# Kernel tuning notes

Hardware: AMD Instinct MI355X
Metric: run time of the kernel (lower is better)

The kernel has to match this reference:

```python
import jax, jax.numpy as jnp
import numpy as np

REPLACE = 4
REMAIN = 32
EPS = 1e-12


def _l2norm(x, axis):
    return x / jnp.maximum(jnp.linalg.norm(x, axis=axis, keepdims=True), EPS)


def setup_inputs() -> dict:
    key = jax.random.key(0)
    ks = jax.random.split(key, 16)
    B, d = 4096, 64
    n_users, n_entities, n_items = 100000, 200000, 50000
    K, n_cans, n_rel = 64, 64, 100
    return {
        "users": jax.random.randint(ks[0], (B,), 0, n_users),
        "items": jax.random.randint(ks[1], (B,), 0, n_items),
        "kg_neighbors": jax.random.randint(ks[2], (n_items, K), 0, n_entities),
        "all_candidates": jax.random.randint(ks[3], (n_rel, n_cans), 0, n_entities),
        "neighbor_relations": jax.random.randint(ks[4], (n_items, K), 0, n_rel),
        "user_all_embeddings": jax.random.normal(ks[5], (n_users, d), jnp.float32),
        "entity_all_embeddings": jax.random.normal(ks[6], (n_entities, d), jnp.float32),
        "item_embeddings": jax.random.normal(ks[7], (B, d), jnp.float32),
        "ui_W": jax.random.normal(ks[8], (2 * d, d), jnp.float32) / np.sqrt(2 * d),
        "ui_b": jnp.zeros((d,), jnp.float32),
        "e1_W": jax.random.normal(ks[9], (d, d), jnp.float32) / np.sqrt(d),
        "e1_b": jnp.zeros((d,), jnp.float32),
        "e2_W": jax.random.normal(ks[10], (d, d), jnp.float32) / np.sqrt(d),
        "e2_b": jnp.zeros((d,), jnp.float32),
    }


def reference(users, items, kg_neighbors, all_candidates, neighbor_relations,
              user_all_embeddings, entity_all_embeddings, item_embeddings,
              ui_W, ui_b, e1_W, e1_b, e2_W, e2_b):
    B = users.shape[0]
    d = user_all_embeddings.shape[1]
    idx_dtype = kg_neighbors.dtype

    neighbors = kg_neighbors[items]                      # [B, K]
    users_e = user_all_embeddings[users]                 # [B, d]
    ui_e = _l2norm(jnp.concatenate([users_e, item_embeddings], axis=1) @ ui_W + ui_b, 1)  # [B, d]

    # Step 1: score neighbors, pick top replace_num
    ne = _l2norm(entity_all_embeddings[neighbors] @ e1_W + e1_b, 2)   # [B, K, d]
    scores1 = jnp.einsum('bd,bkd->bk', ui_e, ne)
    logits1 = jax.nn.softmax(scores1, axis=1)
    step1_prob, step1_idx = jax.lax.top_k(logits1, REPLACE)          # [B, R]
    replaced = jnp.take_along_axis(neighbors, step1_idx, axis=1)     # [B, R]
    sel_rel = jnp.take_along_axis(neighbor_relations[items], step1_idx, axis=1)
    cf_kg1 = kg_neighbors.at[items[:, None], step1_idx].set(
        jnp.zeros((B, REPLACE), idx_dtype))
    ap1 = jnp.log(jnp.mean(step1_prob, axis=1))                      # [B]

    # Step 2: candidate pruning + sampling
    cands = all_candidates[sel_rel]                                  # [B, R, C]
    cands_e = entity_all_embeddings[cands]                           # [B, R, C, d]
    scores2 = jnp.einsum('bd,brcd->brc', users_e, cands_e)
    _, remain_idx = jax.lax.top_k(scores2, REMAIN)                   # [B, R, M]
    cands = jnp.take_along_axis(cands, remain_idx, axis=2).reshape(B * REPLACE, REMAIN)

    replaced_e = _l2norm(entity_all_embeddings[replaced] @ e1_W + e1_b, 2)
    replaced_e = replaced_e.reshape(B * REPLACE, d)
    cands_e2 = _l2norm(entity_all_embeddings[cands] @ e2_W + e2_b, 2)  # [BR, M, d]
    ui_rep = jnp.repeat(ui_e, REPLACE, axis=0)                         # [BR, d]
    s2 = jnp.einsum('nd,nmd->nm', ui_rep * replaced_e, cands_e2)       # [BR, M]
    logp2 = jax.nn.log_softmax(s2, axis=1)

    skey = jax.random.key(42)
    step2_idx = jax.random.categorical(skey, logp2, axis=1)           # [BR]
    rows = jnp.arange(B * REPLACE)
    step2_prob = jnp.exp(logp2[rows, step2_idx]).reshape(B, REPLACE)
    sel_ent = cands[rows, step2_idx].reshape(B, REPLACE)
    cf_kg2 = kg_neighbors.at[items[:, None], step1_idx].set(sel_ent.astype(idx_dtype))
    ap2 = jnp.log(jnp.mean(step1_prob, axis=1)) + jnp.log(jnp.mean(step2_prob, axis=1))
    return (cf_kg1, ap1, cf_kg2, ap2)
```

## Files before the change

### kernel.cpp

```cpp
#include <hip/hip_runtime.h>
#include <stdint.h>

#define EPS_NORM 1e-12f
#define F32_TINY 1.17549435e-38f

static __device__ __forceinline__ int rfl(int v) {
  return __builtin_amdgcn_readfirstlane(v);
}

__device__ __forceinline__ void threefry2x32(uint32_t k0, uint32_t k1,
                                             uint32_t x0, uint32_t x1,
                                             uint32_t& o0, uint32_t& o1) {
  uint32_t ks2 = k0 ^ k1 ^ 0x1BD11BDAu;
  x0 += k0; x1 += k1;
#define TF_ROT(r) { x0 += x1; x1 = (x1 << (r)) | (x1 >> (32 - (r))); x1 ^= x0; }
  TF_ROT(13) TF_ROT(15) TF_ROT(26) TF_ROT(6)
  x0 += k1; x1 += ks2 + 1u;
  TF_ROT(17) TF_ROT(29) TF_ROT(16) TF_ROT(24)
  x0 += ks2; x1 += k0 + 2u;
  TF_ROT(13) TF_ROT(15) TF_ROT(26) TF_ROT(6)
  x0 += k0; x1 += k1 + 3u;
  TF_ROT(17) TF_ROT(29) TF_ROT(16) TF_ROT(24)
  x0 += k1; x1 += ks2 + 4u;
  TF_ROT(13) TF_ROT(15) TF_ROT(26) TF_ROT(6)
  x0 += ks2; x1 += k0 + 5u;
#undef TF_ROT
  o0 = x0; o1 = x1;
}

#define PERM_IDX(p) ((((p) & 7) << 3) | ((p) >> 3))

__global__ __launch_bounds__(256) void k_phase1(
    const float* __restrict__ E, const int* __restrict__ allc,
    const float* __restrict__ W1, const float* __restrict__ b1,
    const float* __restrict__ W2, const float* __restrict__ b2,
    const float* __restrict__ U, const int* __restrict__ users,
    const float* __restrict__ Iemb, const float* __restrict__ uiW,
    const float* __restrict__ uib, const int* __restrict__ kg,
    float* __restrict__ T1, float* __restrict__ T2c,
    float* __restrict__ uiE, float* __restrict__ out0, float* __restrict__ out2,
    int* __restrict__ wkg2) {
  __shared__ float SM[8192];
  const int blk = blockIdx.x, tid = threadIdx.x;
  const int wv = tid >> 6, lane = tid & 63;
  const int NT1B = 782, NT2B = 25, NUIB = 256;
  if (blk < NT1B + NT2B) {
    const bool isT1 = blk < NT1B;
    {
      const float* W = isT1 ? W1 : W2;
      for (int idx = tid; idx < 4096; idx += 256) {
        int k = idx >> 6, c = idx & 63;
        int cg = c & 7, ci = c >> 3;
        SM[k * 64 + ((ci >> 2) * 8 + cg) * 4 + (ci & 3)] = W[idx];
      }
    }
    __syncthreads();
    const int rg = lane >> 3, cg = lane & 7;
    const int sub = lane >> 5, r = lane & 31;
    const float* bias = isT1 ? b1 : b2;
    float bv[8];
#pragma unroll
    for (int ci = 0; ci < 8; ++ci) bv[ci] = bias[ci * 8 + cg];
    float* eTw = SM + 4096 + wv * 1024;
    const float4* eT4 = reinterpret_cast<const float4*>(eTw);
    const float4* W4 = reinterpret_cast<const float4*>(SM);
#pragma unroll 1
    for (int t = 0; t < 2; ++t) {
      int batch = (isT1 ? blk : blk - NT1B) * 2 + t;
      int rbase = batch * 128 + wv * 32;
      if (isT1 && rbase >= 200000) continue;
      int srow = isT1 ? (rbase + r) : allc[rbase + r];
      const float4* Er = reinterpret_cast<const float4*>(E + (size_t)srow * 64);
      float4 a0 = Er[sub * 4 + 0], a1 = Er[sub * 4 + 1];
      float4 a2 = Er[sub * 4 + 2], a3 = Er[sub * 4 + 3];
      float4 a4 = Er[8 + sub * 4 + 0], a5 = Er[8 + sub * 4 + 1];
      float4 a6 = Er[8 + sub * 4 + 2], a7 = Er[8 + sub * 4 + 3];
      float y[4][8];
#pragma unroll
      for (int ri = 0; ri < 4; ++ri)
#pragma unroll
        for (int ci = 0; ci < 8; ++ci) y[ri][ci] = 0.f;
      {
        float ev[16] = {a0.x, a0.y, a0.z, a0.w, a1.x, a1.y, a1.z, a1.w,
                        a2.x, a2.y, a2.z, a2.w, a3.x, a3.y, a3.z, a3.w};
#pragma unroll
        for (int kk = 0; kk < 16; ++kk)
          eTw[(sub * 16 + kk) * 32 + r] = ev[kk];
#pragma unroll 8
        for (int kk = 0; kk < 32; ++kk) {
          float4 e4 = eT4[kk * 8 + rg];
          float4 wa = W4[kk * 16 + cg];
          float4 wb = W4[kk * 16 + 8 + cg];
          float ev4[4] = {e4.x, e4.y, e4.z, e4.w};
          float wv8[8] = {wa.x, wa.y, wa.z, wa.w, wb.x, wb.y, wb.z, wb.w};
#pragma unroll
          for (int ri = 0; ri < 4; ++ri)
#pragma unroll
            for (int ci = 0; ci < 8; ++ci)
              y[ri][ci] = fmaf(ev4[ri], wv8[ci], y[ri][ci]);
        }
      }
      {
        float ev[16] = {a4.x, a4.y, a4.z, a4.w, a5.x, a5.y, a5.z, a5.w,
                        a6.x, a6.y, a6.z, a6.w, a7.x, a7.y, a7.z, a7.w};
#pragma unroll
        for (int kk = 0; kk < 16; ++kk)
          eTw[(sub * 16 + kk) * 32 + r] = ev[kk];
#pragma unroll 8
        for (int kk = 0; kk < 32; ++kk) {
          float4 e4 = eT4[kk * 8 + rg];
          float4 wa = W4[(32 + kk) * 16 + cg];
          float4 wb = W4[(32 + kk) * 16 + 8 + cg];
          float ev4[4] = {e4.x, e4.y, e4.z, e4.w};
          float wv8[8] = {wa.x, wa.y, wa.z, wa.w, wb.x, wb.y, wb.z, wb.w};
#pragma unroll
          for (int ri = 0; ri < 4; ++ri)
#pragma unroll
            for (int ci = 0; ci < 8; ++ci)
              y[ri][ci] = fmaf(ev4[ri], wv8[ci], y[ri][ci]);
        }
      }
#pragma unroll
      for (int ri = 0; ri < 4; ++ri)
#pragma unroll
        for (int ci = 0; ci < 8; ++ci)
          y[ri][ci] = __fadd_rn(y[ri][ci], bv[ci]);
#pragma unroll
      for (int ri = 0; ri < 4; ++ri) {
        float A0 = __fadd_rn(__fmul_rn(y[ri][0], y[ri][0]),
                             __fmul_rn(y[ri][4], y[ri][4]));
        float A1 = __fadd_rn(__fmul_rn(y[ri][1], y[ri][1]),
                             __fmul_rn(y[ri][5], y[ri][5]));
        float A2 = __fadd_rn(__fmul_rn(y[ri][2], y[ri][2]),
                             __fmul_rn(y[ri][6], y[ri][6]));
        float A3 = __fadd_rn(__fmul_rn(y[ri][3], y[ri][3]),
                             __fmul_rn(y[ri][7], y[ri][7]));
        float B0 = __fadd_rn(A0, A2), B1 = __fadd_rn(A1, A3);
        float C = __fadd_rn(B0, B1);
        C = __fadd_rn(C, __shfl_xor(C, 4));
        C = __fadd_rn(C, __shfl_xor(C, 2));
        C = __fadd_rn(C, __shfl_xor(C, 1));
        float denom = fmaxf(sqrtf(C), EPS_NORM);
        int row = rbase + rg * 4 + ri;
        if (isT1) {
          float4* drow = reinterpret_cast<float4*>(T1 + (size_t)row * 64 + cg * 8);
          drow[0] = make_float4(y[ri][0] / denom, y[ri][1] / denom,
                                y[ri][2] / denom, y[ri][3] / denom);
          drow[1] = make_float4(y[ri][4] / denom, y[ri][5] / denom,
                                y[ri][6] / denom, y[ri][7] / denom);
        } else {
          float* drow = T2c + (size_t)row * 64;
#pragma unroll
          for (int ci = 0; ci < 8; ++ci) drow[ci * 8 + cg] = y[ri][ci] / denom;
        }
      }
    }
  } else if (blk < NT1B + NT2B + NUIB) {
    int ub = blk - (NT1B + NT2B);
    for (int i = tid; i < 8192; i += 256) SM[i] = uiW[i];
    __syncthreads();
    float bl = uib[lane];
#pragma unroll 1
    for (int t = 0; t < 4; ++t) {
      int b = ub * 16 + wv * 4 + t;
      int usr = rfl(users[b]);
      const float* ur = U + (size_t)usr * 64;
      const float* ir = Iemb + (size_t)b * 64;
      float y = 0.f;
#pragma unroll
      for (int k = 0; k < 64; ++k) y = fmaf(ur[k], SM[k * 64 + lane], y);
#pragma unroll
      for (int k = 0; k < 64; ++k) y = fmaf(ir[k], SM[(64 + k) * 64 + lane], y);
      y += bl;
      float ss = y * y;
#pragma unroll
      for (int off = 32; off; off >>= 1) ss += __shfl_xor(ss, off);
      float yn = y / fmaxf(sqrtf(ss), EPS_NORM);
      uiE[(size_t)b * 64 + lane] = yn;
    }
  } else {
    const int4* kg4 = reinterpret_cast<const int4*>(kg);
    float4* o4 = reinterpret_cast<float4*>(out0);
    float4* o24 = reinterpret_cast<float4*>(out2);
    int4* wz = reinterpret_cast<int4*>(wkg2);
    int4 z; z.x = 0; z.y = 0; z.z = 0; z.w = 0;
    for (int i = (blk - 1063) * 256 + tid; i < 800000; i += 200 * 256) {
      int4 v = kg4[i];
      float4 f = make_float4((float)v.x, (float)v.y, (float)v.z, (float)v.w);
      o4[i] = f;
      o24[i] = f;
      wz[i] = z;
    }
  }
}

__global__ __launch_bounds__(256) void k_step(
    const int* __restrict__ items, const int* __restrict__ users,
    const int* __restrict__ kg, const int* __restrict__ nrel,
    const int* __restrict__ allc, const float* __restrict__ E,
    const float* __restrict__ T1, const float* __restrict__ T2c,
    const float* __restrict__ uiE, const float* __restrict__ U,
    float* __restrict__ out0, float* __restrict__ ap1_out,
    int* __restrict__ s1i_g, float* __restrict__ lmp1,
    float* __restrict__ p2, int* __restrict__ wkg2) {
  __shared__ int s1_idx_sh[4], s1_rel_sh[4], s1_ent_sh[4];
  __shared__ int kept_sh[128];
  const int tid = threadIdx.x, wv = tid >> 6, lane = tid & 63;
  const int b = blockIdx.x;
  const int item = rfl(items[b]);
  if (wv == 0) {
    int nb = kg[(size_t)item * 64 + lane];
    const float4* R = reinterpret_cast<const float4*>(T1 + (size_t)nb * 64);
    float yn[64];
#pragma unroll
    for (int p4 = 0; p4 < 16; ++p4) {
      float4 v = R[p4];
      yn[PERM_IDX(4 * p4 + 0)] = v.x;
      yn[PERM_IDX(4 * p4 + 1)] = v.y;
      yn[PERM_IDX(4 * p4 + 2)] = v.z;
      yn[PERM_IDX(4 * p4 + 3)] = v.w;
    }
    const float4* Ur = reinterpret_cast<const float4*>(uiE + (size_t)b * 64);
    float D[32];
#pragma unroll
    for (int i4 = 0; i4 < 8; ++i4) {
      float4 ua = Ur[i4], ub = Ur[i4 + 8];
      float uav[4] = {ua.x, ua.y, ua.z, ua.w};
      float ubv[4] = {ub.x, ub.y, ub.z, ub.w};
#pragma unroll
      for (int t = 0; t < 4; ++t) {
        int i = i4 * 4 + t;
        D[i] = __fadd_rn(__fmul_rn(yn[i], uav[t]), __fmul_rn(yn[i + 32], ubv[t]));
      }
    }
#pragma unroll
    for (int i = 0; i < 16; ++i) D[i] = __fadd_rn(D[i], D[i + 16]);
#pragma unroll
    for (int i = 0; i < 8; ++i)  D[i] = __fadd_rn(D[i], D[i + 8]);
#pragma unroll
    for (int i = 0; i < 4; ++i)  D[i] = __fadd_rn(D[i], D[i + 4]);
#pragma unroll
    for (int i = 0; i < 2; ++i)  D[i] = __fadd_rn(D[i], D[i + 2]);
    float s = __fadd_rn(D[0], D[1]);
    float m = s;
#pragma unroll
    for (int off = 32; off; off >>= 1) m = fmaxf(m, __shfl_xor(m, off));
    float ex = expf(s - m);
    float sum = ex;
#pragma unroll
    for (int off = 32; off; off >>= 1) sum += __shfl_xor(sum, off);
    float p = ex / sum;
    int rank = 0;
    for (int k2 = 0; k2 < 64; ++k2) {
      float pv = __shfl(p, k2);
      rank += (pv > p || (pv == p && k2 < lane)) ? 1 : 0;
    }
    float acc = 0.f;
#pragma unroll
    for (int rr = 0; rr < 4; ++rr) {
      unsigned long long msk = __ballot(rank == rr);
      int src = __ffsll(msk) - 1;
      acc += __shfl(p, src);
    }
    float lm = logf(acc * 0.25f);
    if (lane == 0) { ap1_out[b] = lm; lmp1[b] = lm; }
    if (rank < 4) {
      s1_idx_sh[rank] = lane;
      s1_ent_sh[rank] = nb;
      s1_rel_sh[rank] = nrel[(size_t)item * 64 + lane];
      s1i_g[b * 4 + rank] = lane;
      out0[(size_t)item * 64 + lane] = 0.0f;
    }
  }
  __syncthreads();
  const int n = b * 4 + wv;
  const int rel = rfl(s1_rel_sh[wv]);
  const int repl = rfl(s1_ent_sh[wv]);
  const int colsel = rfl(s1_idx_sh[wv]);
  {
    int usr = rfl(users[b]);
    int ent = allc[rel * 64 + lane];
    const float* ur = U + (size_t)usr * 64;
    const float4* e4 = reinterpret_cast<const float4*>(E + (size_t)ent * 64);
    float s = 0.f;
#pragma unroll
    for (int j4 = 0; j4 < 16; ++j4) {
      float4 t = e4[j4];
      s = fmaf(ur[4 * j4 + 0], t.x, s);
      s = fmaf(ur[4 * j4 + 1], t.y, s);
      s = fmaf(ur[4 * j4 + 2], t.z, s);
      s = fmaf(ur[4 * j4 + 3], t.w, s);
    }
    int rank = 0;
    for (int k2 = 0; k2 < 64; ++k2) {
      float sv = __shfl(s, k2);
      rank += (sv > s || (sv == s && k2 < lane)) ? 1 : 0;
    }
    if (rank < 32) kept_sh[wv * 32 + rank] = (lane << 18) | ent;
  }
  {
    int m = lane & 31;
    int pk = kept_sh[wv * 32 + m];
    int c = pk >> 18;
    int ent = pk & 0x3FFFF;
    float q = uiE[(size_t)b * 64 + PERM_IDX(lane)] * T1[(size_t)repl * 64 + lane];
    const float4* c4 = reinterpret_cast<const float4*>(
        T2c + ((size_t)rel * 64 + c) * 64);
    float s = 0.f;
#pragma unroll
    for (int j4 = 0; j4 < 16; ++j4) {
      float4 t = c4[j4];
      s = fmaf(__shfl(q, PERM_IDX(4 * j4 + 0)), t.x, s);
      s = fmaf(__shfl(q, PERM_IDX(4 * j4 + 1)), t.y, s);
      s = fmaf(__shfl(q, PERM_IDX(4 * j4 + 2)), t.z, s);
      s = fmaf(__shfl(q, PERM_IDX(4 * j4 + 3)), t.w, s);
    }
    float mx = s;
#pragma unroll
    for (int off = 1; off < 32; off <<= 1) mx = fmaxf(mx, __shfl_xor(mx, off));
    float shv = s - mx;
    float se = expf(shv);
    float sum = se;
#pragma unroll
    for (int off = 1; off < 32; off <<= 1) sum += __shfl_xor(sum, off);
    float logp = shv - logf(sum);
    uint32_t h0, h1;
    threefry2x32(0u, 42u, 0u, (uint32_t)(n * 32 + m), h0, h1);
    uint32_t bits = h0 ^ h1;
    float u0 = __uint_as_float((bits >> 9) | 0x3F800000u) - 1.0f;
    float uu = fmaxf(u0, F32_TINY);
    float g = -logf(-logf(uu));
    float z = g + logp;
    float bz = z; int bm = m;
#pragma unroll
    for (int off = 1; off < 32; off <<= 1) {
      float oz = __shfl_xor(bz, off);
      int om = __shfl_xor(bm, off);
      if (oz > bz || (oz == bz && om < bm)) { bz = oz; bm = om; }
    }
    if (lane == bm) {
      p2[n] = expf(logp);
      atomicMax(&wkg2[(size_t)item * 64 + colsel], ((b + 1) << 18) | ent);
    }
  }
}

__global__ __launch_bounds__(256) void k_fin2(
    const int* __restrict__ items, const int* __restrict__ s1_idx,
    const int* __restrict__ wkg2, const float* __restrict__ p2,
    const float* __restrict__ lmp1,
    float* __restrict__ out2, float* __restrict__ out3, int N, int B) {
  int i = blockIdx.x * 256 + threadIdx.x;
  if (i < N) {
    int b = i >> 2;
    int item = items[b];
    int col = s1_idx[i];
    int v = wkg2[(size_t)item * 64 + col];
    out2[(size_t)item * 64 + col] = (float)(v & 0x3FFFF);
  }
  if (i < B) {
    float a = ((p2[i * 4] + p2[i * 4 + 1]) + p2[i * 4 + 2]) + p2[i * 4 + 3];
    out3[i] = lmp1[i] + logf(a * 0.25f);
  }
}

__global__ __launch_bounds__(256) void k_init(const int* __restrict__ kg,
                                              float* __restrict__ out0,
                                              int* __restrict__ wkg2, int n) {
  int i = blockIdx.x * 256 + threadIdx.x;
  if (i < n) { int v = kg[i]; out0[i] = (float)v; wkg2[i] = v; }
}

__device__ __forceinline__ void transform_row(const float4* __restrict__ Er,
                                              const float* __restrict__ W,
                                              const float* __restrict__ bias,
                                              float (&yn)[64]) {
  float y[64];
#pragma unroll
  for (int j = 0; j < 64; ++j) y[j] = 0.f;
  float4 c0 = Er[0], c1 = Er[1], c2 = Er[2], c3 = Er[3];
#pragma unroll 1
  for (int cc = 0; cc < 4; ++cc) {
    float4 n0, n1, n2, n3;
    if (cc < 3) { n0 = Er[cc * 4 + 4]; n1 = Er[cc * 4 + 5];
                  n2 = Er[cc * 4 + 6]; n3 = Er[cc * 4 + 7]; }
    float ev[16] = {c0.x, c0.y, c0.z, c0.w, c1.x, c1.y, c1.z, c1.w,
                    c2.x, c2.y, c2.z, c2.w, c3.x, c3.y, c3.z, c3.w};
#pragma unroll
    for (int k2i = 0; k2i < 16; ++k2i) {
      const float4* Wr = reinterpret_cast<const float4*>(
          W + ((size_t)(cc * 16 + k2i)) * 64);
      float ek = ev[k2i];
#pragma unroll
      for (int j4 = 0; j4 < 16; ++j4) {
        float4 w = Wr[j4];
        y[j4 * 4 + 0] = fmaf(ek, w.x, y[j4 * 4 + 0]);
        y[j4 * 4 + 1] = fmaf(ek, w.y, y[j4 * 4 + 1]);
        y[j4 * 4 + 2] = fmaf(ek, w.z, y[j4 * 4 + 2]);
        y[j4 * 4 + 3] = fmaf(ek, w.w, y[j4 * 4 + 3]);
      }
    }
    c0 = n0; c1 = n1; c2 = n2; c3 = n3;
  }
  const float4* B4 = reinterpret_cast<const float4*>(bias);
#pragma unroll
  for (int j4 = 0; j4 < 16; ++j4) {
    float4 bb = B4[j4];
    float bv[4] = {bb.x, bb.y, bb.z, bb.w};
#pragma unroll
    for (int t = 0; t < 4; ++t) y[j4 * 4 + t] = __fadd_rn(y[j4 * 4 + t], bv[t]);
  }
  float S1[32];
#pragma unroll
  for (int i = 0; i < 32; ++i)
    S1[i] = __fadd_rn(__fmul_rn(y[i], y[i]), __fmul_rn(y[i + 32], y[i + 32]));
#pragma unroll
  for (int i = 0; i < 16; ++i) S1[i] = __fadd_rn(S1[i], S1[i + 16]);
#pragma unroll
  for (int i = 0; i < 8; ++i)  S1[i] = __fadd_rn(S1[i], S1[i + 8]);
#pragma unroll
  for (int i = 0; i < 4; ++i)  S1[i] = __fadd_rn(S1[i], S1[i + 4]);
#pragma unroll
  for (int i = 0; i < 2; ++i)  S1[i] = __fadd_rn(S1[i], S1[i + 2]);
  float ss = __fadd_rn(S1[0], S1[1]);
  float denom = fmaxf(sqrtf(ss), EPS_NORM);
// ... 192 lines not shown
  uint32_t bits = h0 ^ h1;
  float u0 = __uint_as_float((bits >> 9) | 0x3F800000u) - 1.0f;
  float uu = fmaxf(u0, F32_TINY);
  float g = -logf(-logf(uu));
  float z = g + logp;
  float bz = z; int bm = m;
#pragma unroll
  for (int off = 1; off < 32; off <<= 1) {
    float oz = __shfl_xor(bz, off);
    int om = __shfl_xor(bm, off);
    if (oz > bz || (oz == bz && om < bm)) { bz = oz; bm = om; }
  }
  if (lane == bm) {
    p2[n] = expf(logp);
    int col = s1_idx[n];
    int item = items[b];
    atomicMax(&wkg2[(size_t)item * 64 + col], ((b + 1) << 18) | ent);
  }
}

__global__ __launch_bounds__(256) void k_sample(
    const int* __restrict__ items,
    const int* __restrict__ s1_idx, const int* __restrict__ s1_rel,
    const int* __restrict__ s1_ent,
    const float* __restrict__ E, const float* __restrict__ W1,
    const float* __restrict__ b1, const float* __restrict__ T2c,
    const float* __restrict__ uiE, const int* __restrict__ kept,
    float* __restrict__ p2, int* __restrict__ wkg2, int N) {
  __shared__ float Wl[4096];
  int tid = threadIdx.x;
  for (int i = tid; i < 4096; i += 256) Wl[i] = W1[i];
  __syncthreads();
  int wid = tid >> 6, lane = tid & 63;
  int n = rfl(blockIdx.x * 4 + wid);
  if (n >= N) return;
  int b = n >> 2;
  int rel = rfl(s1_rel[n]);
  int repl = rfl(s1_ent[n]);
  const float* er = E + (size_t)repl * 64;
  float y = 0.f;
#pragma unroll
  for (int k2 = 0; k2 < 64; ++k2) y = fmaf(er[k2], Wl[k2 * 64 + lane], y);
  y += b1[lane];
  float ss = y * y;
#pragma unroll
  for (int off = 32; off; off >>= 1) ss += __shfl_xor(ss, off);
  float yn = y / fmaxf(sqrtf(ss), EPS_NORM);
  float q = uiE[(size_t)b * 64 + lane] * yn;
  sample_body<false>(q, n, b, lane, items, s1_idx, rel, T2c, kept, p2, wkg2);
}

__global__ __launch_bounds__(256) void k_fin(const int* __restrict__ wkg2,
                                             const float* __restrict__ p2,
                                             const float* __restrict__ lmp1,
                                             float* __restrict__ out2,
                                             float* __restrict__ out3,
                                             int n, int B) {
  int i = blockIdx.x * 256 + threadIdx.x;
  if (i < n) out2[i] = (float)(wkg2[i] & 0x3FFFF);
  if (i < B) {
    float a = ((p2[i * 4] + p2[i * 4 + 1]) + p2[i * 4 + 2]) + p2[i * 4 + 3];
    out3[i] = lmp1[i] + logf(a * 0.25f);
  }
}

extern "C" void kernel_launch(void* const* d_in, const int* in_sizes, int n_in,
                              void* d_out, int out_size, void* d_ws, size_t ws_size,
                              hipStream_t stream) {
  const int*   users = (const int*)d_in[0];
  const int*   items = (const int*)d_in[1];
  const int*   kg    = (const int*)d_in[2];
  const int*   allc  = (const int*)d_in[3];
  const int*   nrel  = (const int*)d_in[4];
  const float* U     = (const float*)d_in[5];
  const float* E     = (const float*)d_in[6];
  const float* Iemb  = (const float*)d_in[7];
  const float* uiW   = (const float*)d_in[8];
  const float* uib   = (const float*)d_in[9];
  const float* e1W   = (const float*)d_in[10];
  const float* e1b   = (const float*)d_in[11];
  const float* e2W   = (const float*)d_in[12];
  const float* e2b   = (const float*)d_in[13];

  const int B = 4096, NCELL = 3200000, NCAND = 6400, NR4 = 16384, NENT = 200000;

  float* out0    = (float*)d_out;
  float* out_ap1 = out0 + NCELL;
  float* out2    = out_ap1 + B;
  float* out_ap2 = out2 + NCELL;

  float* T2c  = (float*)d_ws;
  float* uiE  = T2c + 409600;
  int*   wkg2 = (int*)(uiE + 262144);
  int*   s1i  = wkg2 + NCELL;
  int*   s1r  = s1i + NR4;
  int*   s1e  = s1r + NR4;
  int*   kept = s1e + NR4;
  float* p2   = (float*)(kept + 524288);
  float* lmp1 = p2 + NR4;
  float* T1   = lmp1 + B;
  const size_t WS_NEED = ((size_t)(T1 + (size_t)NENT * 64) - (size_t)d_ws);
  const bool pathA = ws_size >= WS_NEED;

  if (pathA) {
    k_phase1<<<1263, 256, 0, stream>>>(E, allc, e1W, e1b, e2W, e2b, U, users,
                                       Iemb, uiW, uib, kg, T1, T2c, uiE,
                                       out0, out2, wkg2);
    k_step<<<B, 256, 0, stream>>>(items, users, kg, nrel, allc, E, T1, T2c,
                                  uiE, U, out0, out_ap1, s1i, lmp1, p2, wkg2);
    k_fin2<<<(NR4 + 255) / 256, 256, 0, stream>>>(items, s1i, wkg2, p2, lmp1,
                                                  out2, out_ap2, NR4, B);
  } else {
    k_init<<<(NCELL + 255) / 256, 256, 0, stream>>>(kg, out0, wkg2, NCELL);
    k_ui<<<(B + 3) / 4, 256, 0, stream>>>(U, users, Iemb, uiW, uib, uiE, B);
    k_transform64<<<(NCAND + 3) / 4, 256, 0, stream>>>(E, allc, e2W, e2b, T2c, NCAND);
    k_score1<<<B / 4, 256, 0, stream>>>(items, kg, nrel, E, e1W, e1b, uiE,
                                        out0, out_ap1, s1i, s1r, s1e, lmp1, wkg2);
    k_score2<<<(NR4 + 3) / 4, 256, 0, stream>>>(users, s1r, U, E, allc, kept, NR4);
    k_sample<<<(NR4 + 3) / 4, 256, 0, stream>>>(items, s1i, s1r, s1e, E, e1W, e1b,
                                                T2c, uiE, kept, p2, wkg2, NR4);
    k_fin<<<(NCELL + 255) / 256, 256, 0, stream>>>(wkg2, p2, lmp1, out2, out_ap2,
                                                   NCELL, B);
  }
}
```

Measured before the change: 135.5 us.

## Compute neighbor e1 transforms on demand instead of precomputing all entities

Removes the precompute of the e1 transform for all 200000 entities (the T1 table) and instead transforms only the 64 neighbors of each batch row inside the step kernel, with two batch rows per block sharing the W1 tile in LDS. The replaced-entity embedding is also recomputed per wave rather than read from T1. This cuts a large table write and read, plus most of phase1's blocks. In exchange it adds redundant matmul work when entities repeat across rows, a larger LDS footprint, and fewer step blocks.

Result: slower. 139.9 us (+3.2%).

```diff
diff --git a/kernel.cpp b/kernel.cpp
--- a/kernel.cpp
+++ b/kernel.cpp
@@ -32,44 +32,36 @@
 
 __global__ __launch_bounds__(256) void k_phase1(
     const float* __restrict__ E, const int* __restrict__ allc,
-    const float* __restrict__ W1, const float* __restrict__ b1,
     const float* __restrict__ W2, const float* __restrict__ b2,
     const float* __restrict__ U, const int* __restrict__ users,
     const float* __restrict__ Iemb, const float* __restrict__ uiW,
     const float* __restrict__ uib, const int* __restrict__ kg,
-    float* __restrict__ T1, float* __restrict__ T2c,
-    float* __restrict__ uiE, float* __restrict__ out0, float* __restrict__ out2,
+    float* __restrict__ T2c, float* __restrict__ uiE,
+    float* __restrict__ out0, float* __restrict__ out2,
     int* __restrict__ wkg2) {
   __shared__ float SM[8192];
   const int blk = blockIdx.x, tid = threadIdx.x;
   const int wv = tid >> 6, lane = tid & 63;
-  const int NT1B = 782, NT2B = 25, NUIB = 256;
-  if (blk < NT1B + NT2B) {
-    const bool isT1 = blk < NT1B;
-    {
-      const float* W = isT1 ? W1 : W2;
-      for (int idx = tid; idx < 4096; idx += 256) {
-        int k = idx >> 6, c = idx & 63;
-        int cg = c & 7, ci = c >> 3;
-        SM[k * 64 + ((ci >> 2) * 8 + cg) * 4 + (ci & 3)] = W[idx];
-      }
+  if (blk < 25) {
+    for (int idx = tid; idx < 4096; idx += 256) {
+      int k = idx >> 6, c = idx & 63;
+      int cg = c & 7, ci = c >> 3;
+      SM[k * 64 + ((ci >> 2) * 8 + cg) * 4 + (ci & 3)] = W2[idx];
     }
     __syncthreads();
     const int rg = lane >> 3, cg = lane & 7;
     const int sub = lane >> 5, r = lane & 31;
-    const float* bias = isT1 ? b1 : b2;
     float bv[8];
 #pragma unroll
-    for (int ci = 0; ci < 8; ++ci) bv[ci] = bias[ci * 8 + cg];
+    for (int ci = 0; ci < 8; ++ci) bv[ci] = b2[ci * 8 + cg];
     float* eTw = SM + 4096 + wv * 1024;
     const float4* eT4 = reinterpret_cast<const float4*>(eTw);
     const float4* W4 = reinterpret_cast<const float4*>(SM);
 #pragma unroll 1
     for (int t = 0; t < 2; ++t) {
-      int batch = (isT1 ? blk : blk - NT1B) * 2 + t;
+      int batch = blk * 2 + t;
       int rbase = batch * 128 + wv * 32;
-      if (isT1 && rbase >= 200000) continue;
-      int srow = isT1 ? (rbase + r) : allc[rbase + r];
+      int srow = allc[rbase + r];
       const float4* Er = reinterpret_cast<const float4*>(E + (size_t)srow * 64);
       float4 a0 = Er[sub * 4 + 0], a1 = Er[sub * 4 + 1];
       float4 a2 = Er[sub * 4 + 2], a3 = Er[sub * 4 + 3];
@@ -141,22 +133,13 @@
         C = __fadd_rn(C, __shfl_xor(C, 2));
         C = __fadd_rn(C, __shfl_xor(C, 1));
         float denom = fmaxf(sqrtf(C), EPS_NORM);
-        int row = rbase + rg * 4 + ri;
-        if (isT1) {
-          float4* drow = reinterpret_cast<float4*>(T1 + (size_t)row * 64 + cg * 8);
-          drow[0] = make_float4(y[ri][0] / denom, y[ri][1] / denom,
-                                y[ri][2] / denom, y[ri][3] / denom);
-          drow[1] = make_float4(y[ri][4] / denom, y[ri][5] / denom,
-                                y[ri][6] / denom, y[ri][7] / denom);
-        } else {
-          float* drow = T2c + (size_t)row * 64;
-#pragma unroll
-          for (int ci = 0; ci < 8; ++ci) drow[ci * 8 + cg] = y[ri][ci] / denom;
-        }
-      }
-    }
-  } else if (blk < NT1B + NT2B + NUIB) {
-    int ub = blk - (NT1B + NT2B);
+        float* drow = T2c + (size_t)(rbase + rg * 4 + ri) * 64;
+#pragma unroll
+        for (int ci = 0; ci < 8; ++ci) drow[ci * 8 + cg] = y[ri][ci] / denom;
+      }
+    }
+  } else if (blk < 281) {
+    int ub = blk - 25;
     for (int i = tid; i < 8192; i += 256) SM[i] = uiW[i];
     __syncthreads();
     float bl = uib[lane];
@@ -184,7 +167,7 @@
     float4* o24 = reinterpret_cast<float4*>(out2);
     int4* wz = reinterpret_cast<int4*>(wkg2);
     int4 z; z.x = 0; z.y = 0; z.z = 0; z.w = 0;
-    for (int i = (blk - 1063) * 256 + tid; i < 800000; i += 200 * 256) {
+    for (int i = (blk - 281) * 256 + tid; i < 800000; i += 200 * 256) {
       int4 v = kg4[i];
       float4 f = make_float4((float)v.x, (float)v.y, (float)v.z, (float)v.w);
       o4[i] = f;
@@ -194,54 +177,138 @@
   }
 }
 
-__global__ __launch_bounds__(256) void k_step(
+__global__ __launch_bounds__(256) void k_step2(
     const int* __restrict__ items, const int* __restrict__ users,
     const int* __restrict__ kg, const int* __restrict__ nrel,
     const int* __restrict__ allc, const float* __restrict__ E,
-    const float* __restrict__ T1, const float* __restrict__ T2c,
-    const float* __restrict__ uiE, const float* __restrict__ U,
+    const float* __restrict__ W1, const float* __restrict__ b1,
+    const float* __restrict__ T2c, const float* __restrict__ uiE,
+    const float* __restrict__ U,
     float* __restrict__ out0, float* __restrict__ ap1_out,
     int* __restrict__ s1i_g, float* __restrict__ lmp1,
     float* __restrict__ p2, int* __restrict__ wkg2) {
-  __shared__ int s1_idx_sh[4], s1_rel_sh[4], s1_ent_sh[4];
-  __shared__ int kept_sh[128];
+  __shared__ float SMW[4096];
+  __shared__ float eTs[4][1024];
+  __shared__ float scores_sh[2][64];
+  __shared__ int s1_idx_sh[2][4], s1_rel_sh[2][4], s1_ent_sh[2][4];
   const int tid = threadIdx.x, wv = tid >> 6, lane = tid & 63;
-  const int b = blockIdx.x;
-  const int item = rfl(items[b]);
-  if (wv == 0) {
+  const int blk = blockIdx.x;
+  for (int idx = tid; idx < 4096; idx += 256) {
+    int k = idx >> 6, c = idx & 63;
+    int cg = c & 7, ci = c >> 3;
+    SMW[k * 64 + ((ci >> 2) * 8 + cg) * 4 + (ci & 3)] = W1[idx];
+  }
+  __syncthreads();
+  {
+    const int slot = wv >> 1, half = wv & 1;
+    const int b = blk * 2 + slot;
+    const int item = rfl(items[b]);
+    const int rg = lane >> 3, cg = lane & 7;
+    const int sub = lane >> 5, r = lane & 31;
+    float bv[8], uv[8];
+#pragma unroll
+    for (int ci = 0; ci < 8; ++ci) bv[ci] = b1[ci * 8 + cg];
+#pragma unroll
+    for (int ci = 0; ci < 8; ++ci) uv[ci] = uiE[(size_t)b * 64 + ci * 8 + cg];
+    float* eTw = eTs[wv];
+    const float4* eT4 = reinterpret_cast<const float4*>(eTw);
+    const float4* W4 = reinterpret_cast<const float4*>(SMW);
+    const int rloc = half * 32;
+    int srow = kg[(size_t)item * 64 + rloc + r];
+    const float4* Er = reinterpret_cast<const float4*>(E + (size_t)srow * 64);
+    float4 a0 = Er[sub * 4 + 0], a1 = Er[sub * 4 + 1];
+    float4 a2 = Er[sub * 4 + 2], a3 = Er[sub * 4 + 3];
+    float4 a4 = Er[8 + sub * 4 + 0], a5 = Er[8 + sub * 4 + 1];
+    float4 a6 = Er[8 + sub * 4 + 2], a7 = Er[8 + sub * 4 + 3];
+    float y[4][8];
+#pragma unroll
+    for (int ri = 0; ri < 4; ++ri)
+#pragma unroll
+      for (int ci = 0; ci < 8; ++ci) y[ri][ci] = 0.f;
+    {
+      float ev[16] = {a0.x, a0.y, a0.z, a0.w, a1.x, a1.y, a1.z, a1.w,
+                      a2.x, a2.y, a2.z, a2.w, a3.x, a3.y, a3.z, a3.w};
+#pragma unroll
+      for (int kk = 0; kk < 16; ++kk)
+        eTw[(sub * 16 + kk) * 32 + r] = ev[kk];
+#pragma unroll 8
+      for (int kk = 0; kk < 32; ++kk) {
+        float4 e4 = eT4[kk * 8 + rg];
+        float4 wa = W4[kk * 16 + cg];
+        float4 wb = W4[kk * 16 + 8 + cg];
+        float ev4[4] = {e4.x, e4.y, e4.z, e4.w};
+        float wv8[8] = {wa.x, wa.y, wa.z, wa.w, wb.x, wb.y, wb.z, wb.w};
+#pragma unroll
+        for (int ri = 0; ri < 4; ++ri)
+#pragma unroll
+          for (int ci = 0; ci < 8; ++ci)
+            y[ri][ci] = fmaf(ev4[ri], wv8[ci], y[ri][ci]);
+      }
+    }
+    {
+      float ev[16] = {a4.x, a4.y, a4.z, a4.w, a5.x, a5.y, a5.z, a5.w,
+                      a6.x, a6.y, a6.z, a6.w, a7.x, a7.y, a7.z, a7.w};
+#pragma unroll
+      for (int kk = 0; kk < 16; ++kk)
+        eTw[(sub * 16 + kk) * 32 + r] = ev[kk];
+#pragma unroll 8
+      for (int kk = 0; kk < 32; ++kk) {
+        float4 e4 = eT4[kk * 8 + rg];
+        float4 wa = W4[(32 + kk) * 16 + cg];
+        float4 wb = W4[(32 + kk) * 16 + 8 + cg];
+        float ev4[4] = {e4.x, e4.y, e4.z, e4.w};
+        float wv8[8] = {wa.x, wa.y, wa.z, wa.w, wb.x, wb.y, wb.z, wb.w};
+#pragma unroll
+        for (int ri = 0; ri < 4; ++ri)
+#pragma unroll
+          for (int ci = 0; ci < 8; ++ci)
+            y[ri][ci] = fmaf(ev4[ri], wv8[ci], y[ri][ci]);
+      }
+    }
+#pragma unroll
+    for (int ri = 0; ri < 4; ++ri)
+#pragma unroll
+      for (int ci = 0; ci < 8; ++ci)
+        y[ri][ci] = __fadd_rn(y[ri][ci], bv[ci]);
+#pragma unroll
+    for (int ri = 0; ri < 4; ++ri) {
+      float A0 = __fadd_rn(__fmul_rn(y[ri][0], y[ri][0]),
+                           __fmul_rn(y[ri][4], y[ri][4]));
+      float A1 = __fadd_rn(__fmul_rn(y[ri][1], y[ri][1]),
+                           __fmul_rn(y[ri][5], y[ri][5]));
+      float A2 = __fadd_rn(__fmul_rn(y[ri][2], y[ri][2]),
+                           __fmul_rn(y[ri][6], y[ri][6]));
+      float A3 = __fadd_rn(__fmul_rn(y[ri][3], y[ri][3]),
+                           __fmul_rn(y[ri][7], y[ri][7]));
+      float B0 = __fadd_rn(A0, A2), B1 = __fadd_rn(A1, A3);
+      float C = __fadd_rn(B0, B1);
+      C = __fadd_rn(C, __shfl_xor(C, 4));
+      C = __fadd_rn(C, __shfl_xor(C, 2));
+      C = __fadd_rn(C, __shfl_xor(C, 1));
+      float denom = fmaxf(sqrtf(C), EPS_NORM);
+      float yn0 = y[ri][0] / denom, yn1 = y[ri][1] / denom;
+      float yn2 = y[ri][2] / denom, yn3 = y[ri][3] / denom;
+      float yn4 = y[ri][4] / denom, yn5 = y[ri][5] / denom;
+      float yn6 = y[ri][6] / denom, yn7 = y[ri][7] / denom;
+      float D0 = __fadd_rn(__fmul_rn(yn0, uv[0]), __fmul_rn(yn4, uv[4]));
+      float D1 = __fadd_rn(__fmul_rn(yn1, uv[1]), __fmul_rn(yn5, uv[5]));
+      float D2 = __fadd_rn(__fmul_rn(yn2, uv[2]), __fmul_rn(yn6, uv[6]));
+      float D3 = __fadd_rn(__fmul_rn(yn3, uv[3]), __fmul_rn(yn7, uv[7]));
+      float t0 = __fadd_rn(D0, D2), t1 = __fadd_rn(D1, D3);
+      float u0 = __fadd_rn(t0, t1);
+      float sF = __fadd_rn(u0, __shfl_xor(u0, 4));
+      sF = __fadd_rn(sF, __shfl_xor(sF, 2));
+      sF = __fadd_rn(sF, __shfl_xor(sF, 1));
+      if (cg == 0) scores_sh[slot][rloc + rg * 4 + ri] = sF;
+    }
+  }
+  __syncthreads();
+  if ((wv & 1) == 0) {
+    const int slot = wv >> 1;
+    const int b = blk * 2 + slot;
+    const int item = rfl(items[b]);
+    float s = scores_sh[slot][lane];
     int nb = kg[(size_t)item * 64 + lane];
-    const float4* R = reinterpret_cast<const float4*>(T1 + (size_t)nb * 64);
-    float yn[64];
-#pragma unroll
-    for (int p4 = 0; p4 < 16; ++p4) {
-      float4 v = R[p4];
-      yn[PERM_IDX(4 * p4 + 0)] = v.x;
-      yn[PERM_IDX(4 * p4 + 1)] = v.y;
-      yn[PERM_IDX(4 * p4 + 2)] = v.z;
-      yn[PERM_IDX(4 * p4 + 3)] = v.w;
-    }
-    const float4* Ur = reinterpret_cast<const float4*>(uiE + (size_t)b * 64);
-    float D[32];
-#pragma unroll
-    for (int i4 = 0; i4 < 8; ++i4) {
-      float4 ua = Ur[i4], ub = Ur[i4 + 8];
-      float uav[4] = {ua.x, ua.y, ua.z, ua.w};
-      float ubv[4] = {ub.x, ub.y, ub.z, ub.w};
-#pragma unroll
-      for (int t = 0; t < 4; ++t) {
-        int i = i4 * 4 + t;
-        D[i] = __fadd_rn(__fmul_rn(yn[i], uav[t]), __fmul_rn(yn[i + 32], ubv[t]));
-      }
-    }
-#pragma unroll
-    for (int i = 0; i < 16; ++i) D[i] = __fadd_rn(D[i], D[i + 16]);
-#pragma unroll
-    for (int i = 0; i < 8; ++i)  D[i] = __fadd_rn(D[i], D[i + 8]);
-#pragma unroll
-    for (int i = 0; i < 4; ++i)  D[i] = __fadd_rn(D[i], D[i + 4]);
-#pragma unroll
-    for (int i = 0; i < 2; ++i)  D[i] = __fadd_rn(D[i], D[i + 2]);
-    float s = __fadd_rn(D[0], D[1]);
     float m = s;
 #pragma unroll
     for (int off = 32; off; off >>= 1) m = fmaxf(m, __shfl_xor(m, off));
@@ -265,82 +332,107 @@
     float lm = logf(acc * 0.25f);
     if (lane == 0) { ap1_out[b] = lm; lmp1[b] = lm; }
     if (rank < 4) {
-      s1_idx_sh[rank] = lane;
-      s1_ent_sh[rank] = nb;
-      s1_rel_sh[rank] = nrel[(size_t)item * 64 + lane];
+      s1_idx_sh[slot][rank] = lane;
+      s1_ent_sh[slot][rank] = nb;
+      s1_rel_sh[slot][rank] = nrel[(size_t)item * 64 + lane];
       s1i_g[b * 4 + rank] = lane;
       out0[(size_t)item * 64 + lane] = 0.0f;
     }
   }
   __syncthreads();
-  const int n = b * 4 + wv;
-  const int rel = rfl(s1_rel_sh[wv]);
-  const int repl = rfl(s1_ent_sh[wv]);
-  const int colsel = rfl(s1_idx_sh[wv]);
-  {
-    int usr = rfl(users[b]);
-    int ent = allc[rel * 64 + lane];
-    const float* ur = U + (size_t)usr * 64;
-    const float4* e4 = reinterpret_cast<const float4*>(E + (size_t)ent * 64);
-    float s = 0.f;
-#pragma unroll
-    for (int j4 = 0; j4 < 16; ++j4) {
-      float4 t = e4[j4];
-      s = fmaf(ur[4 * j4 + 0], t.x, s);
-      s = fmaf(ur[4 * j4 + 1], t.y, s);
-      s = fmaf(ur[4 * j4 + 2], t.z, s);
-      s = fmaf(ur[4 * j4 + 3], t.w, s);
-    }
-    int rank = 0;
-    for (int k2 = 0; k2 < 64; ++k2) {
-      float sv = __shfl(s, k2);
-      rank += (sv > s || (sv == s && k2 < lane)) ? 1 : 0;
-    }
-    if (rank < 32) kept_sh[wv * 32 + rank] = (lane << 18) | ent;
-  }
-  {
-    int m = lane & 31;
-    int pk = kept_sh[wv * 32 + m];
-    int c = pk >> 18;
-    int ent = pk & 0x3FFFF;
-    float q = uiE[(size_t)b * 64 + PERM_IDX(lane)] * T1[(size_t)repl * 64 + lane];
-    const float4* c4 = reinterpret_cast<const float4*>(
-        T2c + ((size_t)rel * 64 + c) * 64);
-    float s = 0.f;
-#pragma unroll
-    for (int j4 = 0; j4 < 16; ++j4) {
-      float4 t = c4[j4];
-      s = fmaf(__shfl(q, PERM_IDX(4 * j4 + 0)), t.x, s);
-      s = fmaf(__shfl(q, PERM_IDX(4 * j4 + 1)), t.y, s);
-      s = fmaf(__shfl(q, PERM_IDX(4 * j4 + 2)), t.z, s);
-      s = fmaf(__shfl(q, PERM_IDX(4 * j4 + 3)), t.w, s);
-    }
-    float mx = s;
-#pragma unroll
-    for (int off = 1; off < 32; off <<= 1) mx = fmaxf(mx, __shfl_xor(mx, off));
-    float shv = s - mx;
-    float se = expf(shv);
-    float sum = se;
-#pragma unroll
-    for (int off = 1; off < 32; off <<= 1) sum += __shfl_xor(sum, off);
-    float logp = shv - logf(sum);
-    uint32_t h0, h1;
-    threefry2x32(0u, 42u, 0u, (uint32_t)(n * 32 + m), h0, h1);
-    uint32_t bits = h0 ^ h1;
-    float u0 = __uint_as_float((bits >> 9) | 0x3F800000u) - 1.0f;
-    float uu = fmaxf(u0, F32_TINY);
-    float g = -logf(-logf(uu));
-    float z = g + logp;
-    float bz = z; int bm = m;
-#pragma unroll
-    for (int off = 1; off < 32; off <<= 1) {
-      float oz = __shfl_xor(bz, off);
-      int om = __shfl_xor(bm, off);
-      if (oz > bz || (oz == bz && om < bm)) { bz = oz; bm = om; }
-    }
-    if (lane == bm) {
-      p2[n] = expf(logp);
-      atomicMax(&wkg2[(size_t)item * 64 + colsel], ((b + 1) << 18) | ent);
+  const int ciL = lane >> 3, cgL = lane & 7;
+  const int p2idx = (ciL >> 2) * 32 + cgL * 4 + (ciL & 3);
+#pragma unroll 1
+  for (int slot = 0; slot < 2; ++slot) {
+    const int b = blk * 2 + slot;
+    const int item = rfl(items[b]);
+    const int n = b * 4 + wv;
+    const int rel = rfl(s1_rel_sh[slot][wv]);
+    const int repl = rfl(s1_ent_sh[slot][wv]);
+    const int colsel = rfl(s1_idx_sh[slot][wv]);
+    int keptv;
+    int kept_pk;
+    {
+      int usr = rfl(users[b]);
+      int ent = allc[rel * 64 + lane];
+      const float* ur = U + (size_t)usr * 64;
+      const float4* e4 = reinterpret_cast<const float4*>(E + (size_t)ent * 64);
+      float s = 0.f;
+#pragma unroll
+      for (int j4 = 0; j4 < 16; ++j4) {
+        float4 t = e4[j4];
+        s = fmaf(ur[4 * j4 + 0], t.x, s);
+        s = fmaf(ur[4 * j4 + 1], t.y, s);
+        s = fmaf(ur[4 * j4 + 2], t.z, s);
+        s = fmaf(ur[4 * j4 + 3], t.w, s);
+      }
+      int rank = 0;
+      for (int k2 = 0; k2 < 64; ++k2) {
+        float sv = __shfl(s, k2);
+        rank += (sv > s || (sv == s && k2 < lane)) ? 1 : 0;
+      }
+      int pk = (lane << 18) | ent;
+      __shared__ int kept_sh[4][64];
+      if (rank < 32) kept_sh[wv][rank] = pk;
+      keptv = 0;
+      kept_pk = 0;
+      kept_pk = kept_sh[wv][lane & 31];
+      (void)keptv;
+    }
+    {
+      const float* er = E + (size_t)repl * 64;
+      float yv = 0.f;
+#pragma unroll
+      for (int k2 = 0; k2 < 64; ++k2)
+        yv = fmaf(er[k2], SMW[k2 * 64 + p2idx], yv);
+      yv += b1[lane];
+      float ss = yv * yv;
+#pragma unroll
+      for (int off = 32; off; off >>= 1) ss += __shfl_xor(ss, off);
+      float yn = yv / fmaxf(sqrtf(ss), EPS_NORM);
+      float q = uiE[(size_t)b * 64 + lane] * yn;
+      int m = lane & 31;
+      int pk = kept_pk;
+      int c = pk >> 18;
+      int ent = pk & 0x3FFFF;
+      const float4* c4 = reinterpret_cast<const float4*>(
+          T2c + ((size_t)rel * 64 + c) * 64);
+      float s = 0.f;
+#pragma unroll
+      for (int j4 = 0; j4 < 16; ++j4) {
+        float4 t = c4[j4];
+        s = fmaf(__shfl(q, 4 * j4 + 0), t.x, s);
+        s = fmaf(__shfl(q, 4 * j4 + 1), t.y, s);
+        s = fmaf(__shfl(q, 4 * j4 + 2), t.z, s);
+        s = fmaf(__shfl(q, 4 * j4 + 3), t.w, s);
+      }
+      float mx = s;
+#pragma unroll
+      for (int off = 1; off < 32; off <<= 1) mx = fmaxf(mx, __shfl_xor(mx, off));
+      float shv = s - mx;
+      float se = expf(shv);
+      float sum = se;
+#pragma unroll
+      for (int off = 1; off < 32; off <<= 1) sum += __shfl_xor(sum, off);
+      float logp = shv - logf(sum);
+      uint32_t h0, h1;
+      threefry2x32(0u, 42u, 0u, (uint32_t)(n * 32 + m), h0, h1);
+      uint32_t bits = h0 ^ h1;
+      float u0f = __uint_as_float((bits >> 9) | 0x3F800000u) - 1.0f;
+      float uu = fmaxf(u0f, F32_TINY);
+      float g = -logf(-logf(uu));
+      float z = g + logp;
+      float bz = z; int bm = m;
+#pragma unroll
+      for (int off = 1; off < 32; off <<= 1) {
+        float oz = __shfl_xor(bz, off);
+        int om = __shfl_xor(bm, off);
+        if (oz > bz || (oz == bz && om < bm)) { bz = oz; bm = om; }
+      }
+      if (lane == bm) {
+        p2[n] = expf(logp);
+        atomicMax(&wkg2[(size_t)item * 64 + colsel], ((b + 1) << 18) | ent);
+      }
     }
   }
 }
@@ -699,7 +791,7 @@
   const float* e2W   = (const float*)d_in[12];
   const float* e2b   = (const float*)d_in[13];
 
-  const int B = 4096, NCELL = 3200000, NCAND = 6400, NR4 = 16384, NENT = 200000;
+  const int B = 4096, NCELL = 3200000, NCAND = 6400, NR4 = 16384;
 
   float* out0    = (float*)d_out;
   float* out_ap1 = out0 + NCELL;
@@ -715,16 +807,15 @@
   int*   kept = s1e + NR4;
   float* p2   = (float*)(kept + 524288);
   float* lmp1 = p2 + NR4;
-  float* T1   = lmp1 + B;
-  const size_t WS_NEED = ((size_t)(T1 + (size_t)NENT * 64) - (size_t)d_ws);
+  const size_t WS_NEED = ((size_t)(lmp1 + B) - (size_t)d_ws);
   const bool pathA = ws_size >= WS_NEED;
 
   if (pathA) {
-    k_phase1<<<1263, 256, 0, stream>>>(E, allc, e1W, e1b, e2W, e2b, U, users,
-                                       Iemb, uiW, uib, kg, T1, T2c, uiE,
-                                       out0, out2, wkg2);
-    k_step<<<B, 256, 0, stream>>>(items, users, kg, nrel, allc, E, T1, T2c,
-                                  uiE, U, out0, out_ap1, s1i, lmp1, p2, wkg2);
+    k_phase1<<<481, 256, 0, stream>>>(E, allc, e2W, e2b, U, users, Iemb,
+                                      uiW, uib, kg, T2c, uiE, out0, out2, wkg2);
+    k_step2<<<B / 2, 256, 0, stream>>>(items, users, kg, nrel, allc, E,
+                                       e1W, e1b, T2c, uiE, U,
+                                       out0, out_ap1, s1i, lmp1, p2, wkg2);
     k_fin2<<<(NR4 + 255) / 256, 256, 0, stream>>>(items, s1i, wkg2, p2, lmp1,
                                                   out2, out_ap2, NR4, B);
   } else {
```

## Process four batch rows per block so all waves do step-1 scoring

Applied to the files above, without the earlier changes.

The step kernel now handles four batch rows per block. Each of the four waves runs the step-1 neighbor scoring and top-k for its own row, instead of wave 0 working while three waves sit idle. After one barrier, each wave loops over the four rows to do its replacement's candidate scoring and sampling. This removes the idle waves in phase one and cuts the block count by four. The cost is a serial four-iteration loop in phase two and fewer blocks to spread across the GPU.

New measurement: 131.9 us (median of 2 runs). 1.03x faster.

```diff
diff --git a/kernel.cpp b/kernel.cpp
--- a/kernel.cpp
+++ b/kernel.cpp
@@ -194,7 +194,7 @@
   }
 }
 
-__global__ __launch_bounds__(256) void k_step(
+__global__ __launch_bounds__(256) void k_step4(
     const int* __restrict__ items, const int* __restrict__ users,
     const int* __restrict__ kg, const int* __restrict__ nrel,
     const int* __restrict__ allc, const float* __restrict__ E,
@@ -203,12 +203,13 @@
     float* __restrict__ out0, float* __restrict__ ap1_out,
     int* __restrict__ s1i_g, float* __restrict__ lmp1,
     float* __restrict__ p2, int* __restrict__ wkg2) {
-  __shared__ int s1_idx_sh[4], s1_rel_sh[4], s1_ent_sh[4];
-  __shared__ int kept_sh[128];
+  __shared__ int s1_idx_sh[4][4], s1_rel_sh[4][4], s1_ent_sh[4][4];
+  __shared__ int kept_sh[4][32];
   const int tid = threadIdx.x, wv = tid >> 6, lane = tid & 63;
-  const int b = blockIdx.x;
-  const int item = rfl(items[b]);
-  if (wv == 0) {
+  const int blk = blockIdx.x;
+  {
+    const int b = blk * 4 + wv;
+    const int item = rfl(items[b]);
     int nb = kg[(size_t)item * 64 + lane];
     const float4* R = reinterpret_cast<const float4*>(T1 + (size_t)nb * 64);
     float yn[64];
@@ -265,82 +266,88 @@
     float lm = logf(acc * 0.25f);
     if (lane == 0) { ap1_out[b] = lm; lmp1[b] = lm; }
     if (rank < 4) {
-      s1_idx_sh[rank] = lane;
-      s1_ent_sh[rank] = nb;
-      s1_rel_sh[rank] = nrel[(size_t)item * 64 + lane];
+      s1_idx_sh[wv][rank] = lane;
+      s1_ent_sh[wv][rank] = nb;
+      s1_rel_sh[wv][rank] = nrel[(size_t)item * 64 + lane];
       s1i_g[b * 4 + rank] = lane;
       out0[(size_t)item * 64 + lane] = 0.0f;
     }
   }
   __syncthreads();
-  const int n = b * 4 + wv;
-  const int rel = rfl(s1_rel_sh[wv]);
-  const int repl = rfl(s1_ent_sh[wv]);
-  const int colsel = rfl(s1_idx_sh[wv]);
-  {
-    int usr = rfl(users[b]);
-    int ent = allc[rel * 64 + lane];
-    const float* ur = U + (size_t)usr * 64;
-    const float4* e4 = reinterpret_cast<const float4*>(E + (size_t)ent * 64);
-    float s = 0.f;
-#pragma unroll
-    for (int j4 = 0; j4 < 16; ++j4) {
-      float4 t = e4[j4];
-      s = fmaf(ur[4 * j4 + 0], t.x, s);
-      s = fmaf(ur[4 * j4 + 1], t.y, s);
-      s = fmaf(ur[4 * j4 + 2], t.z, s);
-      s = fmaf(ur[4 * j4 + 3], t.w, s);
-    }
-    int rank = 0;
-    for (int k2 = 0; k2 < 64; ++k2) {
-      float sv = __shfl(s, k2);
-      rank += (sv > s || (sv == s && k2 < lane)) ? 1 : 0;
-    }
-    if (rank < 32) kept_sh[wv * 32 + rank] = (lane << 18) | ent;
-  }
-  {
-    int m = lane & 31;
-    int pk = kept_sh[wv * 32 + m];
-    int c = pk >> 18;
-    int ent = pk & 0x3FFFF;
-    float q = uiE[(size_t)b * 64 + PERM_IDX(lane)] * T1[(size_t)repl * 64 + lane];
-    const float4* c4 = reinterpret_cast<const float4*>(
-        T2c + ((size_t)rel * 64 + c) * 64);
-    float s = 0.f;
-#pragma unroll
-    for (int j4 = 0; j4 < 16; ++j4) {
-      float4 t = c4[j4];
-      s = fmaf(__shfl(q, PERM_IDX(4 * j4 + 0)), t.x, s);
-      s = fmaf(__shfl(q, PERM_IDX(4 * j4 + 1)), t.y, s);
-      s = fmaf(__shfl(q, PERM_IDX(4 * j4 + 2)), t.z, s);
-      s = fmaf(__shfl(q, PERM_IDX(4 * j4 + 3)), t.w, s);
-    }
-    float mx = s;
-#pragma unroll
-    for (int off = 1; off < 32; off <<= 1) mx = fmaxf(mx, __shfl_xor(mx, off));
-    float shv = s - mx;
-    float se = expf(shv);
-    float sum = se;
-#pragma unroll
-    for (int off = 1; off < 32; off <<= 1) sum += __shfl_xor(sum, off);
-    float logp = shv - logf(sum);
-    uint32_t h0, h1;
-    threefry2x32(0u, 42u, 0u, (uint32_t)(n * 32 + m), h0, h1);
-    uint32_t bits = h0 ^ h1;
-    float u0 = __uint_as_float((bits >> 9) | 0x3F800000u) - 1.0f;
-    float uu = fmaxf(u0, F32_TINY);
-    float g = -logf(-logf(uu));
-    float z = g + logp;
-    float bz = z; int bm = m;
-#pragma unroll
-    for (int off = 1; off < 32; off <<= 1) {
-      float oz = __shfl_xor(bz, off);
-      int om = __shfl_xor(bm, off);
-      if (oz > bz || (oz == bz && om < bm)) { bz = oz; bm = om; }
-    }
-    if (lane == bm) {
-      p2[n] = expf(logp);
-      atomicMax(&wkg2[(size_t)item * 64 + colsel], ((b + 1) << 18) | ent);
+#pragma unroll 1
+  for (int slot = 0; slot < 4; ++slot) {
+    const int b = blk * 4 + slot;
+    const int item = rfl(items[b]);
+    const int n = b * 4 + wv;
+    const int rel = rfl(s1_rel_sh[slot][wv]);
+    const int repl = rfl(s1_ent_sh[slot][wv]);
+    const int colsel = rfl(s1_idx_sh[slot][wv]);
+    {
+      int usr = rfl(users[b]);
+      int ent = allc[rel * 64 + lane];
+      const float* ur = U + (size_t)usr * 64;
+      const float4* e4 = reinterpret_cast<const float4*>(E + (size_t)ent * 64);
+      float s = 0.f;
+#pragma unroll
+      for (int j4 = 0; j4 < 16; ++j4) {
+        float4 t = e4[j4];
+        s = fmaf(ur[4 * j4 + 0], t.x, s);
+        s = fmaf(ur[4 * j4 + 1], t.y, s);
+        s = fmaf(ur[4 * j4 + 2], t.z, s);
+        s = fmaf(ur[4 * j4 + 3], t.w, s);
+      }
+      int rank = 0;
+      for (int k2 = 0; k2 < 64; ++k2) {
+        float sv = __shfl(s, k2);
+        rank += (sv > s || (sv == s && k2 < lane)) ? 1 : 0;
+      }
+      if (rank < 32) kept_sh[wv][rank] = (lane << 18) | ent;
+    }
+    {
+      int m = lane & 31;
+      int pk = kept_sh[wv][m];
+      int c = pk >> 18;
+      int ent = pk & 0x3FFFF;
+      float q = uiE[(size_t)b * 64 + PERM_IDX(lane)] *
+                T1[(size_t)repl * 64 + lane];
+      const float4* c4 = reinterpret_cast<const float4*>(
+          T2c + ((size_t)rel * 64 + c) * 64);
+      float s = 0.f;
+#pragma unroll
+      for (int j4 = 0; j4 < 16; ++j4) {
+        float4 t = c4[j4];
+        s = fmaf(__shfl(q, PERM_IDX(4 * j4 + 0)), t.x, s);
+        s = fmaf(__shfl(q, PERM_IDX(4 * j4 + 1)), t.y, s);
+        s = fmaf(__shfl(q, PERM_IDX(4 * j4 + 2)), t.z, s);
+        s = fmaf(__shfl(q, PERM_IDX(4 * j4 + 3)), t.w, s);
+      }
+      float mx = s;
+#pragma unroll
+      for (int off = 1; off < 32; off <<= 1) mx = fmaxf(mx, __shfl_xor(mx, off));
+      float shv = s - mx;
+      float se = expf(shv);
+      float sum = se;
+#pragma unroll
+      for (int off = 1; off < 32; off <<= 1) sum += __shfl_xor(sum, off);
+      float logp = shv - logf(sum);
+      uint32_t h0, h1;
+      threefry2x32(0u, 42u, 0u, (uint32_t)(n * 32 + m), h0, h1);
+      uint32_t bits = h0 ^ h1;
+      float u0 = __uint_as_float((bits >> 9) | 0x3F800000u) - 1.0f;
+      float uu = fmaxf(u0, F32_TINY);
+      float g = -logf(-logf(uu));
+      float z = g + logp;
+      float bz = z; int bm = m;
+#pragma unroll
+      for (int off = 1; off < 32; off <<= 1) {
+        float oz = __shfl_xor(bz, off);
+        int om = __shfl_xor(bm, off);
+        if (oz > bz || (oz == bz && om < bm)) { bz = oz; bm = om; }
+      }
+      if (lane == bm) {
+        p2[n] = expf(logp);
+        atomicMax(&wkg2[(size_t)item * 64 + colsel], ((b + 1) << 18) | ent);
+      }
     }
   }
 }
@@ -723,8 +730,8 @@
     k_phase1<<<1263, 256, 0, stream>>>(E, allc, e1W, e1b, e2W, e2b, U, users,
                                        Iemb, uiW, uib, kg, T1, T2c, uiE,
                                        out0, out2, wkg2);
-    k_step<<<B, 256, 0, stream>>>(items, users, kg, nrel, allc, E, T1, T2c,
-                                  uiE, U, out0, out_ap1, s1i, lmp1, p2, wkg2);
+    k_step4<<<B / 4, 256, 0, stream>>>(items, users, kg, nrel, allc, E, T1, T2c,
+                                       uiE, U, out0, out_ap1, s1i, lmp1, p2, wkg2);
     k_fin2<<<(NR4 + 255) / 256, 256, 0, stream>>>(items, s1i, wkg2, p2, lmp1,
                                                   out2, out_ap2, NR4, B);
   } else {
```
